# Kernel tuning notes

Measured on AMD Instinct MI355X. Metric: run time of the kernel, lower is better.

## Reference

```python
import jax, jax.numpy as jnp
import numpy as np
import math

V, D, H, L, DFF = 32000, 512, 8, 6, 1024
DH = D // H
B, S = 8, 1024


def setup_inputs() -> dict:
    key = jax.random.key(0)
    ks = jax.random.split(key, 20)
    x = jax.random.randint(ks[0], (B, S), 0, V, dtype=jnp.int32)
    mask = jnp.zeros((B, 1, S), dtype=bool)
    s = 0.02
    emb = jax.random.normal(ks[1], (V, D), jnp.float32) * s
    Wq = jax.random.normal(ks[2], (L, D, D), jnp.float32) * s
    bq = jnp.zeros((L, D), jnp.float32)
    Wk = jax.random.normal(ks[3], (L, D, D), jnp.float32) * s
    bk = jnp.zeros((L, D), jnp.float32)
    Wv = jax.random.normal(ks[4], (L, D, D), jnp.float32) * s
    bv = jnp.zeros((L, D), jnp.float32)
    Wo = jax.random.normal(ks[5], (L, D, D), jnp.float32) * s
    bo = jnp.zeros((L, D), jnp.float32)
    W1 = jax.random.normal(ks[6], (L, D, DFF), jnp.float32) * s
    b1 = jnp.zeros((L, DFF), jnp.float32)
    W2 = jax.random.normal(ks[7], (L, DFF, D), jnp.float32) * s
    b2 = jnp.zeros((L, D), jnp.float32)
    g1 = jnp.ones((L, D), jnp.float32)
    be1 = jnp.zeros((L, D), jnp.float32)
    g2 = jnp.ones((L, D), jnp.float32)
    be2 = jnp.zeros((L, D), jnp.float32)
    return dict(x=x, mask=mask, emb=emb, Wq=Wq, bq=bq, Wk=Wk, bk=bk, Wv=Wv, bv=bv,
                Wo=Wo, bo=bo, W1=W1, b1=b1, W2=W2, b2=b2, g1=g1, be1=be1, g2=g2, be2=be2)


def _layernorm(x, g, b, eps=1e-5):
    mu = jnp.mean(x, axis=-1, keepdims=True)
    var = jnp.mean(jnp.square(x - mu), axis=-1, keepdims=True)
    return (x - mu) * jax.lax.rsqrt(var + eps) * g + b


def _pos_encoding(seq_len, d_model, dtype):
    pos = jnp.arange(seq_len, dtype=jnp.float32)[:, None]
    div = jnp.exp(jnp.arange(0, d_model, 2, dtype=jnp.float32) * (-math.log(10000.0) / d_model))
    pe = jnp.zeros((seq_len, d_model), jnp.float32)
    pe = pe.at[:, 0::2].set(jnp.sin(pos * div))
    pe = pe.at[:, 1::2].set(jnp.cos(pos * div))
    return pe.astype(dtype)


def _encoder(x, mask, emb, Wq, bq, Wk, bk, Wv, bv, Wo, bo, W1, b1, W2, b2, g1, be1, g2, be2):
    Bs, Ss = x.shape
    h = emb[x] * jnp.asarray(math.sqrt(D), emb.dtype)  # [B,S,D]
    h = h + _pos_encoding(Ss, D, h.dtype)[None]
    # dropout: eval mode (identity)
    m = mask[:, None, :, :]  # [B,1,1,S], True = masked
    for l in range(L):
        q = (h @ Wq[l] + bq[l]).reshape(Bs, Ss, H, DH).transpose(0, 2, 1, 3)
        k = (h @ Wk[l] + bk[l]).reshape(Bs, Ss, H, DH).transpose(0, 2, 1, 3)
        v = (h @ Wv[l] + bv[l]).reshape(Bs, Ss, H, DH).transpose(0, 2, 1, 3)
        logits = jnp.einsum('bhqd,bhkd->bhqk', q, k) / jnp.asarray(math.sqrt(DH), h.dtype)
        logits = jnp.where(m, jnp.asarray(-1e9, h.dtype), logits)
        attn = jax.nn.softmax(logits, axis=-1)
        o = jnp.einsum('bhqk,bhkd->bhqd', attn, v)
        o = o.transpose(0, 2, 1, 3).reshape(Bs, Ss, D)
        o = o @ Wo[l] + bo[l]
        h = _layernorm(h + o, g1[l], be1[l])
        f = jax.nn.relu(h @ W1[l] + b1[l]) @ W2[l] + b2[l]
        h = _layernorm(h + f, g2[l], be2[l])
    return h


def reference(x, mask, emb, Wq, bq, Wk, bk, Wv, bv, Wo, bo, W1, b1, W2, b2, g1, be1, g2, be2):
    return _encoder(x, mask, emb, Wq, bq, Wk, bk, Wv, bv, Wo, bo, W1, b1, W2, b2, g1, be1, g2, be2)
```

## Files before the change

kernel.cpp:

```cpp
#include <hip/hip_runtime.h>
#include <hip/hip_bf16.h>
#include <math.h>

#define BV   8
#define SV   1024
#define DV   512
#define HV   8
#define LV   6
#define DFFV 1024
#define MV   (BV*SV)
#define DHV  64

typedef __attribute__((ext_vector_type(8))) short short8;
typedef __attribute__((ext_vector_type(4))) float f32x4;

__device__ __forceinline__ unsigned short f2b(float f) {
    unsigned u = __float_as_uint(f);
    u = (u + 0x7FFFu + ((u >> 16) & 1u)) >> 16;
    return (unsigned short)u;
}

__device__ __forceinline__ unsigned pk2(float a, float b) {
    union { __hip_bfloat162 h; unsigned u; } cv;
    cv.h = __float22bfloat162_rn(make_float2(a, b));
    return cv.u;
}

__device__ __forceinline__ void async16(const void* g, void* l) {
    __builtin_amdgcn_global_load_lds(
        (const __attribute__((address_space(1))) void*)g,
        (__attribute__((address_space(3))) void*)l, 16, 0, 0);
}

__device__ __forceinline__ f32x4 mfma16(short8 a, short8 b, f32x4 c) {
    return __builtin_amdgcn_mfma_f32_16x16x32_bf16(a, b, c, 0, 0, 0);
}

__device__ __forceinline__ size_t fragaddr(int row, int col, int Kc) {
    return ((size_t)(row >> 4) * (Kc >> 5) + (col >> 5)) * 512
         + (size_t)((row & 15) * 8 + ((col >> 3) & 3) * 128 + (col & 7));
}

__global__ __launch_bounds__(256) void transpose_cvt(
    const float* __restrict__ src, unsigned short* __restrict__ dst,
    int K, int N, long long sstride, long long dstride)
{
    __shared__ float tb[32][33];
    src += (size_t)blockIdx.z * sstride;
    dst += (size_t)blockIdx.z * dstride;
    int n0 = blockIdx.x * 32, k0 = blockIdx.y * 32;
    int tx = threadIdx.x & 31, ty = threadIdx.x >> 5;
    #pragma unroll
    for (int i = 0; i < 4; ++i)
        tb[ty + i * 8][tx] = src[(size_t)(k0 + ty + i * 8) * N + n0 + tx];
    __syncthreads();
    #pragma unroll
    for (int i = 0; i < 4; ++i) {
        int n = n0 + ty + i * 8, k = k0 + tx;
        dst[fragaddr(n, k, K)] = f2b(tb[tx][ty + i * 8]);
    }
}

__global__ __launch_bounds__(256) void pack_bias(
    const float* __restrict__ bq, const float* __restrict__ bk,
    const float* __restrict__ bv, float* __restrict__ bqkv)
{
    int ll = blockIdx.x;
    for (int i = threadIdx.x; i < 1536; i += 256) {
        float v = (i < 512) ? bq[ll * 512 + i]
                : (i < 1024) ? bk[ll * 512 + i - 512]
                             : bv[ll * 512 + i - 1024];
        bqkv[ll * 1536 + i] = v;
    }
}

__global__ __launch_bounds__(256) void embed_pe_kernel(
    const int* __restrict__ x, const float* __restrict__ emb,
    float* __restrict__ h, unsigned short* __restrict__ hb)
{
    int row = blockIdx.x;
    int s   = row & (SV - 1);
    int tok = x[row];
    const float* e  = emb + (size_t)tok * DV;
    float*       hr = h   + (size_t)row * DV;
    for (int d = threadIdx.x; d < DV; d += 256) {
        float v  = e[d] * 22.627416997969522f;
        int   i  = d >> 1;
        float ang = (float)s * __expf(-(float)(2 * i) * (9.210340371976184f / 512.0f));
        float pe  = (d & 1) ? __cosf(ang) : __sinf(ang);
        float o = v + pe;
        hr[d] = o;
        hb[fragaddr(row, d, DV)] = f2b(o);
    }
}

#define OUT_F32 0
#define OUT_B16 1
#define OUT_QKV 2

__global__ __launch_bounds__(256, 2) void gemm_mfma(
    const unsigned short* __restrict__ A,
    const unsigned short* __restrict__ Wt,
    const float* __restrict__ bias,
    int K, int N, int relu, int mode,
    float* __restrict__ Cf, unsigned short* __restrict__ Cb,
    unsigned short* __restrict__ vfr, unsigned short* __restrict__ kfr)
{
    __shared__ unsigned short lds[2][16384];
    const int m0 = blockIdx.x * 128, n0 = blockIdx.y * 128;
    const int t = threadIdx.x, lane = t & 63, w = t >> 6;
    const int l15 = lane & 15, quad = lane >> 4;
    const int mh = w & 1, nh = w >> 1;
    const int kb = K >> 5;

    const unsigned short* gA[4]; const unsigned short* gB[4];
    int oA[4], oB[4];
    #pragma unroll
    for (int i = 0; i < 4; ++i) {
        int blkid = 4 * w + i;
        int msub = blkid >> 1, kd = blkid & 1;
        gA[i] = A  + ((size_t)(m0 / 16 + msub) * kb + kd) * 512 + lane * 8;
        gB[i] = Wt + ((size_t)(n0 / 16 + msub) * kb + kd) * 512 + lane * 8;
        oA[i] = blkid * 512;
        oB[i] = 8192 + blkid * 512;
    }

    f32x4 acc[4][4];
    #pragma unroll
    for (int i = 0; i < 4; ++i)
        #pragma unroll
        for (int j = 0; j < 4; ++j) acc[i][j] = (f32x4){0.f, 0.f, 0.f, 0.f};

    const int nk = K >> 6;

    auto stage = [&](unsigned short* lbuf, int ktile) {
        size_t off = (size_t)ktile * 1024;
        #pragma unroll
        for (int i = 0; i < 4; ++i) {
            async16(gA[i] + off, lbuf + oA[i]);
            async16(gB[i] + off, lbuf + oB[i]);
        }
    };
    auto compute = [&](const unsigned short* lcur) {
        #pragma unroll
        for (int kd = 0; kd < 2; ++kd) {
            short8 af[4], bfr[4];
            #pragma unroll
            for (int i = 0; i < 4; ++i)
                af[i] = *(const short8*)&lcur[((mh * 4 + i) * 2 + kd) * 512 + lane * 8];
            #pragma unroll
            for (int j = 0; j < 4; ++j)
                bfr[j] = *(const short8*)&lcur[8192 + ((nh * 4 + j) * 2 + kd) * 512 + lane * 8];
            #pragma unroll
            for (int i = 0; i < 4; ++i)
                #pragma unroll
                for (int j = 0; j < 4; ++j)
                    acc[i][j] = mfma16(af[i], bfr[j], acc[i][j]);
        }
    };

    stage(lds[0], 0);
    __syncthreads();
    for (int kt = 0; kt < nk; kt += 2) {
        if (kt + 1 < nk) stage(lds[1], kt + 1);
        compute(lds[0]);
        __syncthreads();
        if (kt + 2 < nk) stage(lds[0], kt + 2);
        compute(lds[1]);
        __syncthreads();
    }

    #pragma unroll
    for (int i = 0; i < 4; ++i) {
        int row = m0 + mh * 64 + i * 16 + quad * 4;
        #pragma unroll
        for (int j = 0; j < 4; ++j) {
            int col = n0 + nh * 64 + j * 16 + l15;
            float bj = bias[col];
            float v0 = acc[i][j][0] + bj, v1 = acc[i][j][1] + bj;
            float v2 = acc[i][j][2] + bj, v3 = acc[i][j][3] + bj;
            if (relu) {
                v0 = fmaxf(v0, 0.f); v1 = fmaxf(v1, 0.f);
                v2 = fmaxf(v2, 0.f); v3 = fmaxf(v3, 0.f);
            }
            if (mode == OUT_F32) {
                Cf[(size_t)(row + 0) * N + col] = v0;
                Cf[(size_t)(row + 1) * N + col] = v1;
                Cf[(size_t)(row + 2) * N + col] = v2;
                Cf[(size_t)(row + 3) * N + col] = v3;
            } else if (mode == OUT_B16) {
                size_t fb = fragaddr(row, col, N);
                Cb[fb + 0]  = f2b(v0);
                Cb[fb + 8]  = f2b(v1);
                Cb[fb + 16] = f2b(v2);
                Cb[fb + 24] = f2b(v3);
            } else {
                int b = row >> 10, r1024 = row & 1023;
                if (col < 1024) {
                    int kind = col >> 9;
                    int c512 = col & 511;
                    int hh = c512 >> 6, ch = c512 & 63;
                    float qs = kind ? 1.0f : 0.125f;
                    unsigned short* dstf = kind ? kfr : Cb;
                    size_t addr =
                        ((size_t)((b * 8 + hh) * 128 + (r1024 >> 4) * 2 + (ch >> 5))) * 512
                        + ((ch >> 3) & 3) * 128 + (r1024 & 15) * 8 + (ch & 7);
                    dstf[addr]      = f2b(v0 * qs);
                    dstf[addr + 8]  = f2b(v1 * qs);
                    dstf[addr + 16] = f2b(v2 * qs);
                    dstf[addr + 24] = f2b(v3 * qs);
                } else {
                    int vc = col - 1024, hh = vc >> 6, dh = vc & 63;
                    int key = r1024;
                    size_t addr =
                        ((size_t)((b * 8 + hh) * 128 + (key >> 5) * 4 + (dh >> 4))) * 512
                        + ((key >> 3) & 3) * 128 + (dh & 15) * 8 + (key & 7);
                    ushort4 pk;
                    pk.x = f2b(v0); pk.y = f2b(v1); pk.z = f2b(v2); pk.w = f2b(v3);
                    *(ushort4*)&vfr[addr] = pk;
                }
            }
        }
    }
}

__global__ __launch_bounds__(1024, 4) void gemm_ln(
    const unsigned short* __restrict__ A,
    const unsigned short* __restrict__ Wt,
    const float* __restrict__ bias,
    const float* __restrict__ hres,
    const float* __restrict__ g, const float* __restrict__ be,
    int K,
    float* __restrict__ dst,
    unsigned short* __restrict__ bdst)
{
    __shared__ float lnred[32][16][2];
    const int m0 = blockIdx.x * 32;
    const int lane = threadIdx.x & 63, w = threadIdx.x >> 6;
    const int l15 = lane & 15, quad = lane >> 4;
    const int kb = K >> 5;
    const unsigned short* aA = A  + (size_t)(m0 >> 4) * kb * 512 + lane * 8;
    const unsigned short* aB = Wt + (size_t)(w * 2)   * kb * 512 + lane * 8;

    f32x4 acc[2][2];
    #pragma unroll
    for (int i = 0; i < 2; ++i)
        #pragma unroll
        for (int j = 0; j < 2; ++j) acc[i][j] = (f32x4){0.f, 0.f, 0.f, 0.f};

    const int nk = K >> 6;
    for (int kt = 0; kt < nk; ++kt) {
        short8 a[2][2], b[2][2];
        #pragma unroll
        for (int i = 0; i < 2; ++i)
            #pragma unroll
            for (int kd = 0; kd < 2; ++kd)
                a[i][kd] = *(const short8*)(aA + ((size_t)i * kb + kt * 2 + kd) * 512);
        #pragma unroll
        for (int j = 0; j < 2; ++j)
            #pragma unroll
            for (int kd = 0; kd < 2; ++kd)
                b[j][kd] = *(const short8*)(aB + ((size_t)j * kb + kt * 2 + kd) * 512);
        #pragma unroll
        for (int kd = 0; kd < 2; ++kd)
            #pragma unroll
            for (int i = 0; i < 2; ++i)
                #pragma unroll
                for (int j = 0; j < 2; ++j)
                    acc[i][j] = mfma16(a[i][kd], b[j][kd], acc[i][j]);
    }

    float u[2][2][4];
    #pragma unroll
    for (int i = 0; i < 2; ++i)
        #pragma unroll
        for (int r = 0; r < 4; ++r) {
            int row = m0 + i * 16 + quad * 4 + r;
            float ps = 0.f, ps2 = 0.f;
            #pragma unroll
            for (int j = 0; j < 2; ++j) {
                int col = w * 32 + j * 16 + l15;
                float uu = hres[(size_t)row * DV + col] + acc[i][j][r] + bias[col];
                u[i][j][r] = uu;
                ps += uu; ps2 += uu * uu;
            }
            #pragma unroll
            for (int m = 1; m < 16; m <<= 1) {
                ps  += __shfl_xor(ps, m);
                ps2 += __shfl_xor(ps2, m);
            }
            if (l15 == 0) {
                lnred[i * 16 + quad * 4 + r][w][0] = ps;
                lnred[i * 16 + quad * 4 + r][w][1] = ps2;
            }
        }
    __syncthreads();
    #pragma unroll
    for (int i = 0; i < 2; ++i)
        #pragma unroll
        for (int r = 0; r < 4; ++r) {
            int rl = i * 16 + quad * 4 + r;
            int row = m0 + rl;
            float S1 = 0.f, S2 = 0.f;
            #pragma unroll
            for (int ww = 0; ww < 16; ++ww) {
                S1 += lnred[rl][ww][0];
                S2 += lnred[rl][ww][1];
            }
            float mu  = S1 * (1.0f / 512.0f);
            float inv = rsqrtf(S2 * (1.0f / 512.0f) - mu * mu + 1e-5f);
            #pragma unroll
            for (int j = 0; j < 2; ++j) {
                int col = w * 32 + j * 16 + l15;
                float on = (u[i][j][r] - mu) * inv * g[col] + be[col];
                dst[(size_t)row * DV + col] = on;
                if (bdst) bdst[fragaddr(row, col, DV)] = f2b(on);
            }
        }
}

__global__ __launch_bounds__(1024, 4) void ffn_ln(
    const unsigned short* __restrict__ hbA,
    const unsigned short* __restrict__ W1t,
    const float* __restrict__ b1,
    const unsigned short* __restrict__ W2t,
    const float* __restrict__ b2,
    const float* __restrict__ hres,
    const float* __restrict__ g, const float* __restrict__ be,
    float* __restrict__ dst,
    unsigned short* __restrict__ bdst)
{
    __shared__ unsigned short f1[32768];
    __shared__ float lnred[32][16][2];
    const int m0 = blockIdx.x * 32;
    const int lane = threadIdx.x & 63, w = threadIdx.x >> 6;
    const int l15 = lane & 15, quad = lane >> 4;

    const int kb1 = 16;
    const unsigned short* aA  = hbA + (size_t)(m0 >> 4) * kb1 * 512 + lane * 8;
    const unsigned short* aB1 = W1t + (size_t)(w * 4) * kb1 * 512 + lane * 8;

    f32x4 acc1[2][4];
    #pragma unroll
    for (int i = 0; i < 2; ++i)
        #pragma unroll
        for (int j = 0; j < 4; ++j) acc1[i][j] = (f32x4){0.f, 0.f, 0.f, 0.f};

    for (int kt = 0; kt < 8; ++kt) {
        short8 a[2][2], b[4][2];
        #pragma unroll
        for (int i = 0; i < 2; ++i)
            #pragma unroll
            for (int kd = 0; kd < 2; ++kd)
                a[i][kd] = *(const short8*)(aA + ((size_t)i * kb1 + kt * 2 + kd) * 512);
        #pragma unroll
        for (int j = 0; j < 4; ++j)
            #pragma unroll
            for (int kd = 0; kd < 2; ++kd)
                b[j][kd] = *(const short8*)(aB1 + ((size_t)j * kb1 + kt * 2 + kd) * 512);
        #pragma unroll
        for (int kd = 0; kd < 2; ++kd)
            #pragma unroll
            for (int i = 0; i < 2; ++i)
                #pragma unroll
                for (int j = 0; j < 4; ++j)
                    acc1[i][j] = mfma16(a[i][kd], b[j][kd], acc1[i][j]);
    }

    #pragma unroll
    for (int i = 0; i < 2; ++i)
        #pragma unroll
        for (int j = 0; j < 4; ++j) {
            int col = w * 64 + j * 16 + l15;
            float bj = b1[col];
            int addr = (i * 32 + (col >> 5)) * 512
                     + ((col >> 3) & 3) * 128 + (quad * 4) * 8 + (col & 7);
            #pragma unroll
            for (int r = 0; r < 4; ++r)
                f1[addr + r * 8] = f2b(fmaxf(acc1[i][j][r] + bj, 0.f));
        }
    __syncthreads();

    const int kb2 = 32;
    const unsigned short* aB2 = W2t + (size_t)(w * 2) * kb2 * 512 + lane * 8;

    f32x4 acc2[2][2];
    #pragma unroll
    for (int i = 0; i < 2; ++i)
        #pragma unroll
        for (int j = 0; j < 2; ++j) acc2[i][j] = (f32x4){0.f, 0.f, 0.f, 0.f};

    for (int kt = 0; kt < 32; ++kt) {
        short8 a[2], b[2];
        #pragma unroll
        for (int i = 0; i < 2; ++i)
            a[i] = *(const short8*)&f1[(i * 32 + kt) * 512 + lane * 8];
        #pragma unroll
        for (int j = 0; j < 2; ++j)
            b[j] = *(const short8*)(aB2 + ((size_t)j * kb2 + kt) * 512);
        #pragma unroll
        for (int i = 0; i < 2; ++i)
            #pragma unroll
            for (int j = 0; j < 2; ++j)
                acc2[i][j] = mfma16(a[i], b[j], acc2[i][j]);
    }

    float u[2][2][4];
    #pragma unroll
    for (int i = 0; i < 2; ++i)
        #pragma unroll
        for (int r = 0; r < 4; ++r) {
            int row = m0 + i * 16 + quad * 4 + r;
            float ps = 0.f, ps2 = 0.f;
            #pragma unroll
            for (int j = 0; j < 2; ++j) {
                int col = w * 32 + j * 16 + l15;
                float uu = hres[(size_t)row * DV + col] + acc2[i][j][r] + b2[col];
                u[i][j][r] = uu;
                ps += uu; ps2 += uu * uu;
            }
            #pragma unroll
            for (int m = 1; m < 16; m <<= 1) {
                ps  += __shfl_xor(ps, m);
                ps2 += __shfl_xor(ps2, m);
            }
            if (l15 == 0) {
                lnred[i * 16 + quad * 4 + r][w][0] = ps;
                lnred[i * 16 + quad * 4 + r][w][1] = ps2;
            }
        }
    __syncthreads();
    #pragma unroll
    for (int i = 0; i < 2; ++i)
        #pragma unroll
        for (int r = 0; r < 4; ++r) {
            int rl = i * 16 + quad * 4 + r;
            int row = m0 + rl;
            float S1 = 0.f, S2 = 0.f;
            #pragma unroll
            for (int ww = 0; ww < 16; ++ww) {
                S1 += lnred[rl][ww][0];
                S2 += lnred[rl][ww][1];
            }
            float mu  = S1 * (1.0f / 512.0f);
            float inv = rsqrtf(S2 * (1.0f / 512.0f) - mu * mu + 1e-5f);
            #pragma unroll
            for (int j = 0; j < 2; ++j) {
                int col = w * 32 + j * 16 + l15;
                float on = (u[i][j][r] - mu) * inv * g[col] + be[col];
                dst[(size_t)row * DV + col] = on;
                if (bdst) bdst[fragaddr(row, col, DV)] = f2b(on);
            }
        }
}

__global__ __launch_bounds__(256) void attn_mfma(
    const unsigned short* __restrict__ qfrag,
    const unsigned short* __restrict__ kfrag,
    const unsigned short* __restrict__ vfrag,
    unsigned short* __restrict__ ob)
{
    __shared__ unsigned short plds[9216];
    const int blk = blockIdx.x;
    const int bh = blk & 63, qt = blk >> 6;
    const int h = bh & 7, b = bh >> 3;
    const int lane = threadIdx.x & 63, w = threadIdx.x >> 6;
    const int l15 = lane & 15, quad = lane >> 4;
    const size_t rowb = (size_t)b * 1024;
    const int q0 = qt * 128 + w * 32;
    const int pw = w * 2304;

    const unsigned short* kfb = kfrag + (size_t)bh * 128 * 512 + lane * 8;
    const unsigned short* vfb = vfrag + (size_t)bh * 128 * 512 + lane * 8;
    const unsigned short* qfb = qfrag + (size_t)bh * 128 * 512 + lane * 8;

    short8 qf[2][2];
    #pragma unroll
    for (int rt = 0; rt < 2; ++rt)
        #pragma unroll
        for (int kd = 0; kd < 2; ++kd)
            qf[rt][kd] = *(const short8*)(qfb + (size_t)((qt * 8 + w * 2 + rt) * 2 + kd) * 512);

    f32x4 O[2][4];
    float lsum[2] = {0.f, 0.f};
    #pragma unroll
    for (int rt = 0; rt < 2; ++rt)
        #pragma unroll
        for (int d = 0; d < 4; ++d) O[rt][d] = (f32x4){0.f, 0.f, 0.f, 0.f};

    short8 kf[2][4][2];
    #pragma unroll
    for (int kt = 0; kt < 4; ++kt)
        #pragma unroll
        for (int kd = 0; kd < 2; ++kd)
            kf[0][kt][kd] = *(const short8*)(kfb + (size_t)(kt * 2 + kd) * 512);

    #pragma unroll 2
    for (int kc = 0; kc < 16; ++kc) {
        const int cur = kc & 1, nxt = cur ^ 1;

        short8 vf[4][2];
        #pragma unroll
        for (int kkc = 0; kkc < 2; ++kkc)
            #pragma unroll
            for (int dsub = 0; dsub < 4; ++dsub)
                vf[dsub][kkc] = *(const short8*)(vfb
                    + (size_t)((kc * 2 + kkc) * 4 + dsub) * 512);
        if (kc < 15) {
            #pragma unroll
            for (int kt = 0; kt < 4; ++kt)
                #pragma unroll
                for (int kd = 0; kd < 2; ++kd)
                    kf[nxt][kt][kd] = *(const short8*)(kfb
                        + (size_t)(((kc + 1) * 4 + kt) * 2 + kd) * 512);
        }

        f32x4 s[2][4];
        #pragma unroll
        for (int rt = 0; rt < 2; ++rt)
            #pragma unroll
            for (int kt = 0; kt < 4; ++kt) {
                f32x4 z = (f32x4){0.f, 0.f, 0.f, 0.f};
                z = mfma16(kf[cur][kt][0], qf[rt][0], z);
                z = mfma16(kf[cur][kt][1], qf[rt][1], z);
                s[rt][kt] = z;
            }
        #pragma unroll
        for (int rt = 0; rt < 2; ++rt)
            #pragma unroll
            for (int kt = 0; kt < 4; ++kt) {
                float e0 = __expf(s[rt][kt][0]);
                float e1 = __expf(s[rt][kt][1]);
                float e2 = __expf(s[rt][kt][2]);
                float e3 = __expf(s[rt][kt][3]);
                lsum[rt] += (e0 + e1) + (e2 + e3);
                *(uint2*)&plds[pw + rt * 1152 + l15 * 72 + kt * 16 + quad * 4] =
                    make_uint2(pk2(e0, e1), pk2(e2, e3));
            }
        short8 pa[2][2];
        #pragma unroll
        for (int rt = 0; rt < 2; ++rt)
            #pragma unroll
            for (int kkc = 0; kkc < 2; ++kkc)
                pa[rt][kkc] = *(const short8*)&plds[pw + rt * 1152 + l15 * 72
                                                    + kkc * 32 + quad * 8];
        #pragma unroll
        for (int dsub = 0; dsub < 4; ++dsub)
            #pragma unroll
            for (int kkc = 0; kkc < 2; ++kkc) {
                O[0][dsub] = mfma16(pa[0][kkc], vf[dsub][kkc], O[0][dsub]);
                O[1][dsub] = mfma16(pa[1][kkc], vf[dsub][kkc], O[1][dsub]);
            }
    }

    #pragma unroll
    for (int rt = 0; rt < 2; ++rt) {
        lsum[rt] += __shfl_xor(lsum[rt], 16);
        lsum[rt] += __shfl_xor(lsum[rt], 32);
    }
    #pragma unroll
    for (int rt = 0; rt < 2; ++rt) {
        float inv[4];
        #pragma unroll
        for (int r = 0; r < 4; ++r)
            inv[r] = 1.0f / __shfl(lsum[rt], quad * 4 + r);
        #pragma unroll
        for (int dsub = 0; dsub < 4; ++dsub)
            #pragma unroll
            for (int r = 0; r < 4; ++r) {
                int row = (int)rowb + q0 + rt * 16 + quad * 4 + r;
                int col = h * 64 + dsub * 16 + l15;
                ob[fragaddr(row, col, DV)] = f2b(O[rt][dsub][r] * inv[r]);
            }
    }
}

extern "C" void kernel_launch(void* const* d_in, const int* in_sizes, int n_in,
                              void* d_out, int out_size, void* d_ws, size_t ws_size,
                              hipStream_t stream) {
    const int*   x    = (const int*)d_in[0];
    const float* emb  = (const float*)d_in[2];
    const float* Wq   = (const float*)d_in[3];
    const float* bq   = (const float*)d_in[4];
    const float* Wk   = (const float*)d_in[5];
    const float* bk   = (const float*)d_in[6];
    const float* Wv   = (const float*)d_in[7];
    const float* bv   = (const float*)d_in[8];
    const float* Wo   = (const float*)d_in[9];
    const float* bo   = (const float*)d_in[10];
    const float* W1   = (const float*)d_in[11];
    const float* b1   = (const float*)d_in[12];
    const float* W2   = (const float*)d_in[13];
    const float* b2   = (const float*)d_in[14];
    const float* g1   = (const float*)d_in[15];
    const float* be1  = (const float*)d_in[16];
    const float* g2   = (const float*)d_in[17];
    const float* be2  = (const float*)d_in[18];

    char* p = (char*)d_ws;
    float* h   = (float*)p;                      p += (size_t)MV * DV * 4;
    float* t32 = (float*)p;                      p += (size_t)MV * DV * 4;
    unsigned short* qfrag = (unsigned short*)t32;
    unsigned short* kfrag = qfrag + (size_t)MV * DV;
    unsigned short* hb   = (unsigned short*)p;   p += (size_t)MV * DV * 2;
    unsigned short* qkb  = (unsigned short*)p;   p += (size_t)MV * 1024 * 2;
    unsigned short* obb  = (unsigned short*)p;   p += (size_t)MV * DV * 2;
    unsigned short* vfrag = (unsigned short*)p;  p += (size_t)MV * DV * 2;
    unsigned short* wqkvt = (unsigned short*)p;  p += (size_t)LV * 1536 * 512 * 2;
    unsigned short* wot   = (unsigned short*)p;  p += (size_t)LV * 512 * 512 * 2;
    unsigned short* w1t   = (unsigned short*)p;  p += (size_t)LV * 1024 * 512 * 2;
    unsigned short* w2t   = (unsigned short*)p;  p += (size_t)LV * 512 * 1024 * 2;
    float* bqkv = (float*)p;                     p += (size_t)LV * 1536 * 4;

    transpose_cvt<<<dim3(16,16,LV), 256, 0, stream>>>(Wq, wqkvt,              512, 512, 512*512, 1536*512);
    transpose_cvt<<<dim3(16,16,LV), 256, 0, stream>>>(Wk, wqkvt + 512*512,    512, 512, 512*512, 1536*512);
    transpose_cvt<<<dim3(16,16,LV), 256, 0, stream>>>(Wv, wqkvt + 1024*512,   512, 512, 512*512, 1536*512);
    transpose_cvt<<<dim3(16,16,LV), 256, 0, stream>>>(Wo, wot, 512, 512, 512*512, 512*512);
    transpose_cvt<<<dim3(32,16,LV), 256, 0, stream>>>(W1, w1t, 512, 1024, 512*1024, 1024*512);
    transpose_cvt<<<dim3(16,32,LV), 256, 0, stream>>>(W2, w2t, 1024, 512, 1024*512, 512*1024);
    pack_bias<<<LV, 256, 0, stream>>>(bq, bk, bv, bqkv);

    embed_pe_kernel<<<MV, 256, 0, stream>>>(x, emb, h, hb);

    for (int l = 0; l < LV; ++l) {
        gemm_mfma<<<dim3(64, 12), 256, 0, stream>>>(
            hb, wqkvt + (size_t)l * 1536 * 512, bqkv + l * 1536,
            512, 1536, 0, OUT_QKV, nullptr, qfrag, vfrag, kfrag);

        attn_mfma<<<512, 256, 0, stream>>>(qfrag, kfrag, vfrag, obb);

        gemm_ln<<<256, 1024, 0, stream>>>(
            obb, wot + (size_t)l * 512 * 512, bo + l * 512,
            h, g1 + l * 512, be1 + l * 512, 512, h, hb);

        float* dst = (l == LV - 1) ? (float*)d_out : h;
        ffn_ln<<<256, 1024, 0, stream>>>(
            hb, w1t + (size_t)l * 1024 * 512, b1 + l * 1024,
            w2t + (size_t)l * 512 * 1024, b2 + l * 512,
            h, g2 + l * 512, be2 + l * 512,
            dst, (l == LV - 1) ? nullptr : hb);
    }
}
```

Baseline: 852.7 us.

## Fuse output projection, LayerNorm1 and FFN into one block-tail kernel

Merges the Wo GEMM plus first residual LayerNorm with the FFN plus second LayerNorm into a single kernel per 32-row tile. The LN1 output stays in registers for the second residual and goes to shared memory in fragment layout as the W1 operand. This removes one launch and the global write and re-read of h/hb between the two kernels. It adds 32 KB of shared memory per block, which may lower occupancy.

```diff
diff --git a/kernel.cpp b/kernel.cpp
--- a/kernel.cpp
+++ b/kernel.cpp
@@ -224,234 +224,214 @@
     }
 }
 
-__global__ __launch_bounds__(1024, 4) void gemm_ln(
-    const unsigned short* __restrict__ A,
-    const unsigned short* __restrict__ Wt,
-    const float* __restrict__ bias,
+__global__ __launch_bounds__(1024, 4) void block_tail(
+    const unsigned short* __restrict__ obb,
+    const unsigned short* __restrict__ wot,
+    const float* __restrict__ bo,
+    const unsigned short* __restrict__ w1t,
+    const float* __restrict__ b1,
+    const unsigned short* __restrict__ w2t,
+    const float* __restrict__ b2,
     const float* __restrict__ hres,
-    const float* __restrict__ g, const float* __restrict__ be,
-    int K,
+    const float* __restrict__ g1, const float* __restrict__ be1,
+    const float* __restrict__ g2, const float* __restrict__ be2,
     float* __restrict__ dst,
     unsigned short* __restrict__ bdst)
 {
-    __shared__ float lnred[32][16][2];
-    const int m0 = blockIdx.x * 32;
-    const int lane = threadIdx.x & 63, w = threadIdx.x >> 6;
-    const int l15 = lane & 15, quad = lane >> 4;
-    const int kb = K >> 5;
-    const unsigned short* aA = A  + (size_t)(m0 >> 4) * kb * 512 + lane * 8;
-    const unsigned short* aB = Wt + (size_t)(w * 2)   * kb * 512 + lane * 8;
-
-    f32x4 acc[2][2];
-    #pragma unroll
-    for (int i = 0; i < 2; ++i)
-        #pragma unroll
-        for (int j = 0; j < 2; ++j) acc[i][j] = (f32x4){0.f, 0.f, 0.f, 0.f};
-
-    const int nk = K >> 6;
-    for (int kt = 0; kt < nk; ++kt) {
-        short8 a[2][2], b[2][2];
-        #pragma unroll
-        for (int i = 0; i < 2; ++i)
-            #pragma unroll
-            for (int kd = 0; kd < 2; ++kd)
-                a[i][kd] = *(const short8*)(aA + ((size_t)i * kb + kt * 2 + kd) * 512);
-        #pragma unroll
-        for (int j = 0; j < 2; ++j)
-            #pragma unroll
-            for (int kd = 0; kd < 2; ++kd)
-                b[j][kd] = *(const short8*)(aB + ((size_t)j * kb + kt * 2 + kd) * 512);
-        #pragma unroll
-        for (int kd = 0; kd < 2; ++kd)
-            #pragma unroll
-            for (int i = 0; i < 2; ++i)
-                #pragma unroll
-                for (int j = 0; j < 2; ++j)
-                    acc[i][j] = mfma16(a[i][kd], b[j][kd], acc[i][j]);
-    }
-
-    float u[2][2][4];
-    #pragma unroll
-    for (int i = 0; i < 2; ++i)
-        #pragma unroll
-        for (int r = 0; r < 4; ++r) {
-            int row = m0 + i * 16 + quad * 4 + r;
-            float ps = 0.f, ps2 = 0.f;
-            #pragma unroll
-            for (int j = 0; j < 2; ++j) {
-                int col = w * 32 + j * 16 + l15;
-                float uu = hres[(size_t)row * DV + col] + acc[i][j][r] + bias[col];
-                u[i][j][r] = uu;
-                ps += uu; ps2 += uu * uu;
-            }
-            #pragma unroll
-            for (int m = 1; m < 16; m <<= 1) {
-                ps  += __shfl_xor(ps, m);
-                ps2 += __shfl_xor(ps2, m);
-            }
-            if (l15 == 0) {
-                lnred[i * 16 + quad * 4 + r][w][0] = ps;
-                lnred[i * 16 + quad * 4 + r][w][1] = ps2;
-            }
-        }
-    __syncthreads();
-    #pragma unroll
-    for (int i = 0; i < 2; ++i)
-        #pragma unroll
-        for (int r = 0; r < 4; ++r) {
-            int rl = i * 16 + quad * 4 + r;
-            int row = m0 + rl;
-            float S1 = 0.f, S2 = 0.f;
-            #pragma unroll
-            for (int ww = 0; ww < 16; ++ww) {
-                S1 += lnred[rl][ww][0];
-                S2 += lnred[rl][ww][1];
-            }
-            float mu  = S1 * (1.0f / 512.0f);
-            float inv = rsqrtf(S2 * (1.0f / 512.0f) - mu * mu + 1e-5f);
-            #pragma unroll
-            for (int j = 0; j < 2; ++j) {
-                int col = w * 32 + j * 16 + l15;
-                float on = (u[i][j][r] - mu) * inv * g[col] + be[col];
-                dst[(size_t)row * DV + col] = on;
-                if (bdst) bdst[fragaddr(row, col, DV)] = f2b(on);
-            }
-        }
-}
-
-__global__ __launch_bounds__(1024, 4) void ffn_ln(
-    const unsigned short* __restrict__ hbA,
-    const unsigned short* __restrict__ W1t,
-    const float* __restrict__ b1,
-    const unsigned short* __restrict__ W2t,
-    const float* __restrict__ b2,
-    const float* __restrict__ hres,
-    const float* __restrict__ g, const float* __restrict__ be,
-    float* __restrict__ dst,
-    unsigned short* __restrict__ bdst)
-{
+    __shared__ unsigned short u1lds[16384];
     __shared__ unsigned short f1[32768];
     __shared__ float lnred[32][16][2];
     const int m0 = blockIdx.x * 32;
     const int lane = threadIdx.x & 63, w = threadIdx.x >> 6;
     const int l15 = lane & 15, quad = lane >> 4;
 
-    const int kb1 = 16;
-    const unsigned short* aA  = hbA + (size_t)(m0 >> 4) * kb1 * 512 + lane * 8;
-    const unsigned short* aB1 = W1t + (size_t)(w * 4) * kb1 * 512 + lane * 8;
-
-    f32x4 acc1[2][4];
-    #pragma unroll
-    for (int i = 0; i < 2; ++i)
-        #pragma unroll
-        for (int j = 0; j < 4; ++j) acc1[i][j] = (f32x4){0.f, 0.f, 0.f, 0.f};
-
-    for (int kt = 0; kt < 8; ++kt) {
-        short8 a[2][2], b[4][2];
-        #pragma unroll
-        for (int i = 0; i < 2; ++i)
+    {
+        const unsigned short* aA  = obb + (size_t)(m0 >> 4) * 16 * 512 + lane * 8;
+        const unsigned short* aBo = wot + (size_t)(w * 2) * 16 * 512 + lane * 8;
+        f32x4 acc[2][2];
+        #pragma unroll
+        for (int i = 0; i < 2; ++i)
+            #pragma unroll
+            for (int j = 0; j < 2; ++j) acc[i][j] = (f32x4){0.f, 0.f, 0.f, 0.f};
+        for (int kt = 0; kt < 8; ++kt) {
+            short8 a[2][2], b[2][2];
+            #pragma unroll
+            for (int i = 0; i < 2; ++i)
+                #pragma unroll
+                for (int kd = 0; kd < 2; ++kd)
+                    a[i][kd] = *(const short8*)(aA + ((size_t)i * 16 + kt * 2 + kd) * 512);
+            #pragma unroll
+            for (int j = 0; j < 2; ++j)
+                #pragma unroll
+                for (int kd = 0; kd < 2; ++kd)
+                    b[j][kd] = *(const short8*)(aBo + ((size_t)j * 16 + kt * 2 + kd) * 512);
             #pragma unroll
             for (int kd = 0; kd < 2; ++kd)
-                a[i][kd] = *(const short8*)(aA + ((size_t)i * kb1 + kt * 2 + kd) * 512);
-        #pragma unroll
-        for (int j = 0; j < 4; ++j)
+                #pragma unroll
+                for (int i = 0; i < 2; ++i)
+                    #pragma unroll
+                    for (int j = 0; j < 2; ++j)
+                        acc[i][j] = mfma16(a[i][kd], b[j][kd], acc[i][j]);
+        }
+        float u[2][2][4];
+        #pragma unroll
+        for (int i = 0; i < 2; ++i)
+            #pragma unroll
+            for (int r = 0; r < 4; ++r) {
+                int row = m0 + i * 16 + quad * 4 + r;
+                float ps = 0.f, ps2 = 0.f;
+                #pragma unroll
+                for (int j = 0; j < 2; ++j) {
+                    int col = w * 32 + j * 16 + l15;
+                    float uu = hres[(size_t)row * DV + col] + acc[i][j][r] + bo[col];
+                    u[i][j][r] = uu;
+                    ps += uu; ps2 += uu * uu;
+                }
+                #pragma unroll
+                for (int m = 1; m < 16; m <<= 1) {
+                    ps  += __shfl_xor(ps, m);
+                    ps2 += __shfl_xor(ps2, m);
+                }
+                if (l15 == 0) {
+                    lnred[i * 16 + quad * 4 + r][w][0] = ps;
+                    lnred[i * 16 + quad * 4 + r][w][1] = ps2;
+                }
+            }
+        __syncthreads();
+        #pragma unroll
+        for (int i = 0; i < 2; ++i)
+            #pragma unroll
+            for (int r = 0; r < 4; ++r) {
+                int rl = i * 16 + quad * 4 + r;
+                float S1 = 0.f, S2 = 0.f;
+                #pragma unroll
+                for (int ww = 0; ww < 16; ++ww) {
+                    S1 += lnred[rl][ww][0];
+                    S2 += lnred[rl][ww][1];
+                }
+                float mu  = S1 * (1.0f / 512.0f);
+                float inv = rsqrtf(S2 * (1.0f / 512.0f) - mu * mu + 1e-5f);
+                #pragma unroll
+                for (int j = 0; j < 2; ++j) {
+                    int col = w * 32 + j * 16 + l15;
+                    float v = (u[i][j][r] - mu) * inv * g1[col] + be1[col];
+                    u[i][j][r] = v;
+                    int addr = (i * 16 + w) * 512
+                             + ((j * 2 + (l15 >> 3)) & 3) * 128
+                             + (quad * 4 + r) * 8 + (l15 & 7);
+                    u1lds[addr] = f2b(v);
+                }
+            }
+        __syncthreads();
+
+        const unsigned short* aB1 = w1t + (size_t)(w * 4) * 16 * 512 + lane * 8;
+        f32x4 acc1[2][4];
+        #pragma unroll
+        for (int i = 0; i < 2; ++i)
+            #pragma unroll
+            for (int j = 0; j < 4; ++j) acc1[i][j] = (f32x4){0.f, 0.f, 0.f, 0.f};
+        for (int kt = 0; kt < 8; ++kt) {
+            short8 a[2][2], b[4][2];
+            #pragma unroll
+            for (int i = 0; i < 2; ++i)
+                #pragma unroll
+                for (int kd = 0; kd < 2; ++kd)
+                    a[i][kd] = *(const short8*)&u1lds[(i * 16 + kt * 2 + kd) * 512 + lane * 8];
+            #pragma unroll
+            for (int j = 0; j < 4; ++j)
+                #pragma unroll
+                for (int kd = 0; kd < 2; ++kd)
+                    b[j][kd] = *(const short8*)(aB1 + ((size_t)j * 16 + kt * 2 + kd) * 512);
             #pragma unroll
             for (int kd = 0; kd < 2; ++kd)
-                b[j][kd] = *(const short8*)(aB1 + ((size_t)j * kb1 + kt * 2 + kd) * 512);
-        #pragma unroll
-        for (int kd = 0; kd < 2; ++kd)
+                #pragma unroll
+                for (int i = 0; i < 2; ++i)
+                    #pragma unroll
+                    for (int j = 0; j < 4; ++j)
+                        acc1[i][j] = mfma16(a[i][kd], b[j][kd], acc1[i][j]);
+        }
+        #pragma unroll
+        for (int i = 0; i < 2; ++i)
+            #pragma unroll
+            for (int j = 0; j < 4; ++j) {
+                int col = w * 64 + j * 16 + l15;
+                float bj = b1[col];
+                int addr = (i * 32 + (col >> 5)) * 512
+                         + ((col >> 3) & 3) * 128 + (quad * 4) * 8 + (col & 7);
+                #pragma unroll
+                for (int r = 0; r < 4; ++r)
+                    f1[addr + r * 8] = f2b(fmaxf(acc1[i][j][r] + bj, 0.f));
+            }
+        __syncthreads();
+
+        const unsigned short* aB2 = w2t + (size_t)(w * 2) * 32 * 512 + lane * 8;
+        f32x4 acc2[2][2];
+        #pragma unroll
+        for (int i = 0; i < 2; ++i)
+            #pragma unroll
+            for (int j = 0; j < 2; ++j) acc2[i][j] = (f32x4){0.f, 0.f, 0.f, 0.f};
+        for (int kt = 0; kt < 32; ++kt) {
+            short8 a[2], b[2];
             #pragma unroll
             for (int i = 0; i < 2; ++i)
-                #pragma unroll
-                for (int j = 0; j < 4; ++j)
-                    acc1[i][j] = mfma16(a[i][kd], b[j][kd], acc1[i][j]);
-    }
-
-    #pragma unroll
-    for (int i = 0; i < 2; ++i)
-        #pragma unroll
-        for (int j = 0; j < 4; ++j) {
-            int col = w * 64 + j * 16 + l15;
-            float bj = b1[col];
-            int addr = (i * 32 + (col >> 5)) * 512
-                     + ((col >> 3) & 3) * 128 + (quad * 4) * 8 + (col & 7);
-            #pragma unroll
-            for (int r = 0; r < 4; ++r)
-                f1[addr + r * 8] = f2b(fmaxf(acc1[i][j][r] + bj, 0.f));
+                a[i] = *(const short8*)&f1[(i * 32 + kt) * 512 + lane * 8];
+            #pragma unroll
+            for (int j = 0; j < 2; ++j)
+                b[j] = *(const short8*)(aB2 + ((size_t)j * 32 + kt) * 512);
+            #pragma unroll
+            for (int i = 0; i < 2; ++i)
+                #pragma unroll
+                for (int j = 0; j < 2; ++j)
+                    acc2[i][j] = mfma16(a[i], b[j], acc2[i][j]);
         }
-    __syncthreads();
-
-    const int kb2 = 32;
-    const unsigned short* aB2 = W2t + (size_t)(w * 2) * kb2 * 512 + lane * 8;
-
-    f32x4 acc2[2][2];
-    #pragma unroll
-    for (int i = 0; i < 2; ++i)
-        #pragma unroll
-        for (int j = 0; j < 2; ++j) acc2[i][j] = (f32x4){0.f, 0.f, 0.f, 0.f};
-
-    for (int kt = 0; kt < 32; ++kt) {
-        short8 a[2], b[2];
-        #pragma unroll
-        for (int i = 0; i < 2; ++i)
-            a[i] = *(const short8*)&f1[(i * 32 + kt) * 512 + lane * 8];
-        #pragma unroll
-        for (int j = 0; j < 2; ++j)
-            b[j] = *(const short8*)(aB2 + ((size_t)j * kb2 + kt) * 512);
-        #pragma unroll
-        for (int i = 0; i < 2; ++i)
-            #pragma unroll
-            for (int j = 0; j < 2; ++j)
-                acc2[i][j] = mfma16(a[i], b[j], acc2[i][j]);
-    }
-
-    float u[2][2][4];
-    #pragma unroll
-    for (int i = 0; i < 2; ++i)
-        #pragma unroll
-        for (int r = 0; r < 4; ++r) {
-            int row = m0 + i * 16 + quad * 4 + r;
-            float ps = 0.f, ps2 = 0.f;
-            #pragma unroll
-            for (int j = 0; j < 2; ++j) {
-                int col = w * 32 + j * 16 + l15;
-                float uu = hres[(size_t)row * DV + col] + acc2[i][j][r] + b2[col];
-                u[i][j][r] = uu;
-                ps += uu; ps2 += uu * uu;
-            }
-            #pragma unroll
-            for (int m = 1; m < 16; m <<= 1) {
-                ps  += __shfl_xor(ps, m);
-                ps2 += __shfl_xor(ps2, m);
-            }
-            if (l15 == 0) {
-                lnred[i * 16 + quad * 4 + r][w][0] = ps;
-                lnred[i * 16 + quad * 4 + r][w][1] = ps2;
-            }
-        }
-    __syncthreads();
-    #pragma unroll
-    for (int i = 0; i < 2; ++i)
-        #pragma unroll
-        for (int r = 0; r < 4; ++r) {
-            int rl = i * 16 + quad * 4 + r;
-            int row = m0 + rl;
-            float S1 = 0.f, S2 = 0.f;
-            #pragma unroll
-            for (int ww = 0; ww < 16; ++ww) {
-                S1 += lnred[rl][ww][0];
-                S2 += lnred[rl][ww][1];
-            }
-            float mu  = S1 * (1.0f / 512.0f);
-            float inv = rsqrtf(S2 * (1.0f / 512.0f) - mu * mu + 1e-5f);
-            #pragma unroll
-            for (int j = 0; j < 2; ++j) {
-                int col = w * 32 + j * 16 + l15;
-                float on = (u[i][j][r] - mu) * inv * g[col] + be[col];
-                dst[(size_t)row * DV + col] = on;
-                if (bdst) bdst[fragaddr(row, col, DV)] = f2b(on);
-            }
-        }
+
+        float u2[2][2][4];
+        #pragma unroll
+        for (int i = 0; i < 2; ++i)
+            #pragma unroll
+            for (int r = 0; r < 4; ++r) {
+                float ps = 0.f, ps2 = 0.f;
+                #pragma unroll
+                for (int j = 0; j < 2; ++j) {
+                    int col = w * 32 + j * 16 + l15;
+                    float uu = u[i][j][r] + acc2[i][j][r] + b2[col];
+                    u2[i][j][r] = uu;
+                    ps += uu; ps2 += uu * uu;
+                }
+                #pragma unroll
+                for (int m = 1; m < 16; m <<= 1) {
+                    ps  += __shfl_xor(ps, m);
+                    ps2 += __shfl_xor(ps2, m);
+                }
+                if (l15 == 0) {
+                    lnred[i * 16 + quad * 4 + r][w][0] = ps;
+                    lnred[i * 16 + quad * 4 + r][w][1] = ps2;
+                }
+            }
+        __syncthreads();
+        #pragma unroll
+        for (int i = 0; i < 2; ++i)
+            #pragma unroll
+            for (int r = 0; r < 4; ++r) {
+                int rl = i * 16 + quad * 4 + r;
+                int row = m0 + rl;
+                float S1 = 0.f, S2 = 0.f;
+                #pragma unroll
+                for (int ww = 0; ww < 16; ++ww) {
+                    S1 += lnred[rl][ww][0];
+                    S2 += lnred[rl][ww][1];
+                }
+                float mu  = S1 * (1.0f / 512.0f);
+                float inv = rsqrtf(S2 * (1.0f / 512.0f) - mu * mu + 1e-5f);
+                #pragma unroll
+                for (int j = 0; j < 2; ++j) {
+                    int col = w * 32 + j * 16 + l15;
+                    float on = (u2[i][j][r] - mu) * inv * g2[col] + be2[col];
+                    dst[(size_t)row * DV + col] = on;
+                    if (bdst) bdst[fragaddr(row, col, DV)] = f2b(on);
+                }
+            }
+    }
 }
 
 __global__ __launch_bounds__(256) void attn_mfma(
@@ -629,15 +609,12 @@
 
         attn_mfma<<<512, 256, 0, stream>>>(qfrag, kfrag, vfrag, obb);
 
-        gemm_ln<<<256, 1024, 0, stream>>>(
+        float* dst = (l == LV - 1) ? (float*)d_out : h;
+        block_tail<<<256, 1024, 0, stream>>>(
             obb, wot + (size_t)l * 512 * 512, bo + l * 512,
-            h, g1 + l * 512, be1 + l * 512, 512, h, hb);
-
-        float* dst = (l == LV - 1) ? (float*)d_out : h;
-        ffn_ln<<<256, 1024, 0, stream>>>(
-            hb, w1t + (size_t)l * 1024 * 512, b1 + l * 1024,
+            w1t + (size_t)l * 1024 * 512, b1 + l * 1024,
             w2t + (size_t)l * 512 * 1024, b2 + l * 512,
-            h, g2 + l * 512, be2 + l * 512,
+            h, g1 + l * 512, be1 + l * 512, g2 + l * 512, be2 + l * 512,
             dst, (l == LV - 1) ? nullptr : hb);
     }
 }
```

Result: faster. 812.8 us (-4.7%).
